# Optimization experiments

Measured on AMD Instinct MI355X. Metric: run time of the kernel, lower is better.

Reference implementation:

```python
import jax, jax.numpy as jnp
import numpy as np

N = 50000
E = 600000
D_IN = 128
HID = 128
OUT = 64


def setup_inputs() -> dict:
    key = jax.random.key(0)
    ks = jax.random.split(key, 12)
    x = jax.random.normal(ks[0], (N, D_IN), dtype=jnp.float32)
    edge_index = jax.random.randint(ks[1], (2, E), 0, N, dtype=jnp.int32)
    def lin(k, fan_in, fan_out):
        lim = 1.0 / np.sqrt(fan_in)
        kw, kb = jax.random.split(k)
        W = jax.random.uniform(kw, (fan_in, fan_out), minval=-lim, maxval=lim, dtype=jnp.float32)
        b = jax.random.uniform(kb, (fan_out,), minval=-lim, maxval=lim, dtype=jnp.float32)
        return W, b
    W1, b1 = lin(ks[2], D_IN, HID)
    W2, b2 = lin(ks[3], HID, HID)
    W3, b3 = lin(ks[4], HID, HID)
    fcW, fcb = lin(ks[5], HID, OUT)
    return {"x": x, "edge_index": edge_index, "W1": W1, "b1": b1,
            "W2": W2, "b2": b2, "W3": W3, "b3": b3, "fcW": fcW, "fcb": fcb}


def _gcn_prep(edge_index):
    # add self loops, compute symmetric normalization deg^-1/2 * deg^-1/2
    loop = jnp.arange(N, dtype=edge_index.dtype)
    src = jnp.concatenate([edge_index[0], loop])
    dst = jnp.concatenate([edge_index[1], loop])
    deg = jax.ops.segment_sum(jnp.ones_like(dst, dtype=jnp.float32), dst, num_segments=N)
    dinv = jnp.where(deg > 0, jax.lax.rsqrt(deg), 0.0)
    norm = dinv[src] * dinv[dst]  # [E+N]
    return src, dst, norm


def _gcn_layer(x, src, dst, norm, W, b):
    h = x @ W                      # [N, F_out]
    msg = h[src] * norm[:, None]   # gather + scale, [E+N, F_out]
    agg = jax.ops.segment_sum(msg, dst, num_segments=N)
    return agg + b


def reference(x, edge_index, W1, b1, W2, b2, W3, b3, fcW, fcb):
    src, dst, norm = _gcn_prep(edge_index)
    x = jax.nn.relu(_gcn_layer(x, src, dst, norm, W1, b1))
    x = jax.nn.relu(_gcn_layer(x, src, dst, norm, W2, b2))
    x = jax.nn.relu(_gcn_layer(x, src, dst, norm, W3, b3))
    virtual_node_embedding = x[-1]  # last node's embedding [HID]
    out = virtual_node_embedding @ fcW + fcb  # [OUT]
    return out
```

## Files before the change

kernel.cpp:

```cpp
#include <hip/hip_runtime.h>

#define NF 128
#define OUTF 64

#define M2 1
#define M1 2
#define M0 4

#define CAP_F2 2048
#define CAP_E3 4096
#define CAP_F1 32768
#define CAP_E2 65536
#define CAP_F0 131072
#define CAP_E1 262144


__global__ void k_seed(int* __restrict__ mark, int* __restrict__ F2,
                       int* __restrict__ cnt, int last) {
    if (threadIdx.x == 0) {
        mark[last] = M2;
        F2[0] = last;
        cnt[0] = 1;
    }
}

__global__ void k_mark(const int* __restrict__ src, const int* __restrict__ dst, int E,
                       int* __restrict__ mark, int checkBit, int setBit, int last,
                       int2* __restrict__ Elist, int Ecap, int* __restrict__ eCnt,
                       int* __restrict__ Flist, int Fcap, int* __restrict__ fCnt,
                       const int* __restrict__ selfList, const int* __restrict__ selfCnt,
                       int selfCap)
{
    int i = blockIdx.x * blockDim.x + threadIdx.x;

    if (selfList) {
        int sc = *selfCnt; if (sc > selfCap) sc = selfCap;
        if (i < sc) {
            int v = selfList[i];
            if (!(atomicOr(&mark[v], setBit) & setBit)) {
                int p = atomicAdd(fCnt, 1);
                if (p < Fcap) Flist[p] = v;
            }
        }
    }
    if (i < E) {
        int d = dst[i];
        bool hit = checkBit ? ((mark[d] & checkBit) != 0) : (d == last);
        if (hit) {
            int s = src[i];
            int p = atomicAdd(eCnt, 1);
            if (p < Ecap) Elist[p] = make_int2(s, d);
            if (!(atomicOr(&mark[s], setBit) & setBit)) {
                int q = atomicAdd(fCnt, 1);
                if (q < Fcap) Flist[q] = s;
            }
        }
    }
}

__global__ void k_degm(const int* __restrict__ dst, const int* __restrict__ mark,
                       int* __restrict__ deg, int E) {
    int i = blockIdx.x * blockDim.x + threadIdx.x;
    if (i < E) {
        int d = dst[i];
        if (mark[d]) atomicAdd(&deg[d], 1);
    }
}

__global__ void k_dinvm(const int* __restrict__ mark, const int* __restrict__ deg,
                        float* __restrict__ dinv, int n) {
    int i = blockIdx.x * blockDim.x + threadIdx.x;
    if (i < n && mark[i]) dinv[i] = rsqrtf(1.0f + (float)deg[i]);
}

__global__ __launch_bounds__(256) void k_gemm_rows(
    const int* __restrict__ list, const int* __restrict__ cntPtr, int cap,
    const float* __restrict__ Xin, const float* __restrict__ bias,
    const float* __restrict__ W, const float* __restrict__ dinv,
    const int* __restrict__ mark, int aggBit, int last,
    float* __restrict__ H, float* __restrict__ AGG)
{
    __shared__ float wsm[128][128];
    const int t = threadIdx.x;

    {
        const float4* W4 = (const float4*)W;
        float4* S4 = (float4*)&wsm[0][0];
        #pragma unroll
        for (int it = 0; it < 16; ++it) S4[it * 256 + t] = W4[it * 256 + t];
    }
    __syncthreads();

    int cnt = *cntPtr; if (cnt > cap) cnt = cap;
    const int wave = t >> 6, lane = t & 63;

    for (int base = blockIdx.x * 4; base < cnt; base += gridDim.x * 4) {
        int r = base + wave;
        if (r >= cnt) continue;
        int v = list[r];
        size_t off = (size_t)v * NF;

        float x0, x1;
        if (bias) {
            x0 = fmaxf(Xin[off + lane]      + bias[lane],      0.f);
            x1 = fmaxf(Xin[off + lane + 64] + bias[lane + 64], 0.f);
        } else {
            x0 = Xin[off + lane];
            x1 = Xin[off + lane + 64];
        }

        float a0 = 0.f, a1 = 0.f;
        #pragma unroll 16
        for (int k = 0; k < 64; ++k) {
            float xk = __shfl(x0, k);
            a0 += xk * wsm[k][lane];
            a1 += xk * wsm[k][lane + 64];
        }
        #pragma unroll 16
        for (int k = 0; k < 64; ++k) {
            float xk = __shfl(x1, k);
            a0 += xk * wsm[k + 64][lane];
            a1 += xk * wsm[k + 64][lane + 64];
        }

        H[off + lane]      = a0;
        H[off + lane + 64] = a1;

        bool doAgg = (mark ? ((mark[v] & aggBit) != 0) : false) || (v == last);
        if (doAgg) {
            float di = dinv[v], s2 = di * di;
            AGG[off + lane]      = a0 * s2;
            AGG[off + lane + 64] = a1 * s2;
        }
    }
}

__global__ void k_scat(const int2* __restrict__ list, const int* __restrict__ cntPtr, int cap,
                       const float* __restrict__ dinv, const float* __restrict__ H,
                       float* __restrict__ AGG)
{
    int cnt = *cntPtr; if (cnt > cap) cnt = cap;
    int t = threadIdx.x;
    for (int i = blockIdx.x; i < cnt; i += gridDim.x) {
        int2 e = list[i];
        float w = dinv[e.x] * dinv[e.y];
        atomicAdd(&AGG[(size_t)e.y * NF + t], H[(size_t)e.x * NF + t] * w);
    }
}

__global__ void k_fc(const float* __restrict__ AGG3, const float* __restrict__ b3,
                     const float* __restrict__ fcW, const float* __restrict__ fcb,
                     float* __restrict__ out, int last)
{
    __shared__ float xrow[NF];
    int j = threadIdx.x;
    size_t off = (size_t)last * NF;
    xrow[j]      = fmaxf(AGG3[off + j]      + b3[j],      0.f);
    xrow[j + 64] = fmaxf(AGG3[off + j + 64] + b3[j + 64], 0.f);
    __syncthreads();
    float acc = fcb[j];
    #pragma unroll 16
    for (int k = 0; k < NF; ++k) acc += xrow[k] * fcW[k * OUTF + j];
    out[j] = acc;
}

extern "C" void kernel_launch(void* const* d_in, const int* in_sizes, int n_in,
                              void* d_out, int out_size, void* d_ws, size_t ws_size,
                              hipStream_t stream)
{
    const float* x    = (const float*)d_in[0];
    const int*   ei   = (const int*)d_in[1];
    const float* W1   = (const float*)d_in[2];
    const float* b1   = (const float*)d_in[3];
    const float* W2   = (const float*)d_in[4];
    const float* b2   = (const float*)d_in[5];
    const float* W3   = (const float*)d_in[6];
    const float* b3   = (const float*)d_in[7];
    const float* fcW  = (const float*)d_in[8];
    const float* fcb  = (const float*)d_in[9];
    float* out = (float*)d_out;

    const int n = in_sizes[0] / NF;
    const int E = in_sizes[1] / 2;
    const int* src = ei;
    const int* dst = ei + E;
    const int last = n - 1;

    char* wp = (char*)d_ws;
    auto alloc = [&](size_t bytes) -> void* {
        void* r = (void*)wp;
        wp += (bytes + 255) & ~(size_t)255;
        return r;
    };
    int*   deg  = (int*)alloc((size_t)n * 4);
    int*   mark = (int*)alloc((size_t)n * 4);
    int*   cnt  = (int*)alloc(64 * 4);
    size_t zbytes = (char*)wp - (char*)deg;

    float* dinv = (float*)alloc((size_t)n * 4);
    int*   F2   = (int*) alloc(CAP_F2 * 4);
    int2*  E3   = (int2*)alloc(CAP_E3 * 8);
    int*   F1   = (int*) alloc(CAP_F1 * 4);
    int2*  E2   = (int2*)alloc(CAP_E2 * 8);
    int*   F0   = (int*) alloc(CAP_F0 * 4);
    int2*  E1   = (int2*)alloc(CAP_E1 * 8);
    float* H    = (float*)alloc((size_t)n * NF * 4);
    float* aggA = (float*)alloc((size_t)n * NF * 4);
    float* aggB = (float*)alloc((size_t)n * NF * 4);

    const int B  = 256;
    const int EB = (E + B - 1) / B;
    const int NB = (n + B - 1) / B;

    hipMemsetAsync(deg, 0, zbytes, stream);
    k_seed<<<1, 64, 0, stream>>>(mark, F2, cnt, last);

    k_mark<<<EB, B, 0, stream>>>(src, dst, E, mark, 0,  M2, last,
                                 E3, CAP_E3, &cnt[1], F2, CAP_F2, &cnt[0],
                                 nullptr, nullptr, 0);
    k_mark<<<EB, B, 0, stream>>>(src, dst, E, mark, M2, M1, last,
                                 E2, CAP_E2, &cnt[3], F1, CAP_F1, &cnt[2],
                                 F2, &cnt[0], CAP_F2);
    k_mark<<<EB, B, 0, stream>>>(src, dst, E, mark, M1, M0, last,
                                 E1, CAP_E1, &cnt[5], F0, CAP_F0, &cnt[4],
                                 F1, &cnt[2], CAP_F1);

    k_degm <<<EB, B, 0, stream>>>(dst, mark, deg, E);
    k_dinvm<<<NB, B, 0, stream>>>(mark, deg, dinv, n);

    k_gemm_rows<<<384, B, 0, stream>>>(F0, &cnt[4], CAP_F0, x, nullptr, W1,
                                       dinv, mark, M1, -1, H, aggA);
    k_scat<<<2048, 128, 0, stream>>>(E1, &cnt[5], CAP_E1, dinv, H, aggA);

    k_gemm_rows<<<384, B, 0, stream>>>(F1, &cnt[2], CAP_F1, aggA, b1, W2,
                                       dinv, mark, M2, -1, H, aggB);
    k_scat<<<2048, 128, 0, stream>>>(E2, &cnt[3], CAP_E2, dinv, H, aggB);

    k_gemm_rows<<<384, B, 0, stream>>>(F2, &cnt[0], CAP_F2, aggB, b2, W3,
                                       dinv, nullptr, 0, last, H, aggA);
    k_scat<<<2048, 128, 0, stream>>>(E3, &cnt[1], CAP_E3, dinv, H, aggA);

    k_fc<<<1, 64, 0, stream>>>(aggA, b3, fcW, fcb, out, last);
}
```

Measured before the change: 166.7 us.

## Fuse all GCN stages into one cooperative persistent kernel with grid syncs

Replaces the sequence of separate launches (memset, BFS marking, degree, gemm, scatter, fc) with a single cooperative kernel that separates the phases with grid-wide syncs. Degree counting is folded into the first BFS pass, dinv is recomputed on the fly with rsqrt instead of being stored, and the final layer plus the fc are done by one block without atomics. This removes per-launch overhead and the extra edge passes. In exchange, grid size is capped at 512 blocks, grid syncs add cost, and the layer-2 and layer-3 gemms read W from global memory instead of LDS.

Measured after the change: 623.4 us. 3.74x slower.

```diff
diff --git a/kernel.cpp b/kernel.cpp
--- a/kernel.cpp
+++ b/kernel.cpp
@@ -1,4 +1,7 @@
 #include <hip/hip_runtime.h>
+#include <hip/hip_cooperative_groups.h>
+
+namespace cg = cooperative_groups;
 
 #define NF 128
 #define OUTF 64
@@ -13,6 +16,243 @@
 #define CAP_E2 65536
 #define CAP_F0 131072
 #define CAP_E1 262144
+
+
+
+struct KArgs {
+    const float* x;
+    const int* srcp;
+    const int* dstp;
+    int E, n, last;
+    const float* W1; const float* b1;
+    const float* W2; const float* b2;
+    const float* W3; const float* b3;
+    const float* fcW; const float* fcb;
+    int* deg; int* mark; int* cnt;
+    int* F2; int2* E3l; int* F1; int2* E2l; int* F0; int2* E1l;
+    float* H; float* aggA; float* aggB;
+    float* out;
+};
+
+__device__ __forceinline__ void bfs_level(
+    const int* __restrict__ src, const int* __restrict__ dst, int E,
+    int* __restrict__ mark, int checkBit, int setBit,
+    int2* __restrict__ Elist, int Ecap, int* __restrict__ eCnt,
+    int* __restrict__ Flist, int Fcap, int* __restrict__ fCnt,
+    const int* __restrict__ selfList, int selfCnt,
+    int gtid, int gstride)
+{
+    for (int i = gtid; i < selfCnt; i += gstride) {
+        int v = selfList[i];
+        if (!(atomicOr(&mark[v], setBit) & setBit)) {
+            int p = atomicAdd(fCnt, 1);
+            if (p < Fcap) Flist[p] = v;
+        }
+    }
+    for (int i = gtid; i < E; i += gstride) {
+        int d = dst[i];
+        if (mark[d] & checkBit) {
+            int s = src[i];
+            int p = atomicAdd(eCnt, 1);
+            if (p < Ecap) Elist[p] = make_int2(s, d);
+            if (!(atomicOr(&mark[s], setBit) & setBit)) {
+                int q = atomicAdd(fCnt, 1);
+                if (q < Fcap) Flist[q] = s;
+            }
+        }
+    }
+}
+
+template<bool USE_LDS>
+__device__ __forceinline__ void gemm_phase(
+    const int* __restrict__ list, int rows,
+    const float* __restrict__ Xin, const float* __restrict__ bias,
+    const float* __restrict__ W, const int* __restrict__ deg,
+    const int* __restrict__ mark, int aggBit,
+    float* __restrict__ H, float* __restrict__ AGG,
+    float (&wsm)[128][128])
+{
+    if ((int)blockIdx.x * 4 >= rows) return;
+    const int t = threadIdx.x;
+    if (USE_LDS) {
+        const float4* W4 = (const float4*)W;
+        float4* S4 = (float4*)&wsm[0][0];
+        #pragma unroll
+        for (int it = 0; it < 16; ++it) S4[it * 256 + t] = W4[it * 256 + t];
+        __syncthreads();
+    }
+    const int wave = t >> 6, lane = t & 63;
+    for (int base = blockIdx.x * 4; base < rows; base += gridDim.x * 4) {
+        int r = base + wave;
+        if (r >= rows) continue;
+        int v = list[r];
+        size_t off = (size_t)v * NF;
+
+        float x0, x1;
+        if (bias) {
+            x0 = fmaxf(Xin[off + lane]      + bias[lane],      0.f);
+            x1 = fmaxf(Xin[off + lane + 64] + bias[lane + 64], 0.f);
+        } else {
+            x0 = Xin[off + lane];
+            x1 = Xin[off + lane + 64];
+        }
+
+        float a0 = 0.f, a1 = 0.f;
+        if (USE_LDS) {
+            #pragma unroll 16
+            for (int k = 0; k < 64; ++k) {
+                float xk = __shfl(x0, k);
+                a0 += xk * wsm[k][lane];
+                a1 += xk * wsm[k][lane + 64];
+            }
+            #pragma unroll 16
+            for (int k = 0; k < 64; ++k) {
+                float xk = __shfl(x1, k);
+                a0 += xk * wsm[k + 64][lane];
+                a1 += xk * wsm[k + 64][lane + 64];
+            }
+        } else {
+            #pragma unroll 8
+            for (int k = 0; k < 64; ++k) {
+                float xk = __shfl(x0, k);
+                a0 += xk * W[k * NF + lane];
+                a1 += xk * W[k * NF + lane + 64];
+            }
+            #pragma unroll 8
+            for (int k = 0; k < 64; ++k) {
+                float xk = __shfl(x1, k);
+                a0 += xk * W[(k + 64) * NF + lane];
+                a1 += xk * W[(k + 64) * NF + lane + 64];
+            }
+        }
+
+        H[off + lane]      = a0;
+        H[off + lane + 64] = a1;
+
+        if (mark[v] & aggBit) {
+            float di = rsqrtf(1.0f + (float)deg[v]);
+            float s2 = di * di;
+            AGG[off + lane]      = a0 * s2;
+            AGG[off + lane + 64] = a1 * s2;
+        }
+    }
+}
+
+__device__ __forceinline__ void scat_phase(
+    const int2* __restrict__ Elist, int ecnt,
+    const int* __restrict__ deg, const float* __restrict__ H,
+    float* __restrict__ AGG, int gtid, int gstride)
+{
+    int grp = gtid >> 7, f = gtid & 127, ngrp = gstride >> 7;
+    for (int i = grp; i < ecnt; i += ngrp) {
+        int2 e = Elist[i];
+        float w = rsqrtf(1.f + (float)deg[e.x]) * rsqrtf(1.f + (float)deg[e.y]);
+        atomicAdd(&AGG[(size_t)e.y * NF + f], H[(size_t)e.x * NF + f] * w);
+    }
+}
+
+__global__ __launch_bounds__(256, 2) void k_fused(KArgs a)
+{
+    __shared__ float wsm[128][128];
+    cg::grid_group grid = cg::this_grid();
+    const int gtid = blockIdx.x * blockDim.x + threadIdx.x;
+    const int gstride = gridDim.x * blockDim.x;
+    const int E = a.E, n = a.n, last = a.last;
+
+    for (int i = gtid; i < n; i += gstride) { a.deg[i] = 0; a.mark[i] = 0; }
+    if (gtid < 64) a.cnt[gtid] = 0;
+    grid.sync();
+
+    if (gtid == 0) {
+        if (!(atomicOr(&a.mark[last], M2) & M2)) {
+            int p = atomicAdd(&a.cnt[0], 1);
+            if (p < CAP_F2) a.F2[p] = last;
+        }
+    }
+    for (int i = gtid; i < E; i += gstride) {
+        int d = a.dstp[i];
+        atomicAdd(&a.deg[d], 1);
+        if (d == last) {
+            int s = a.srcp[i];
+            int p = atomicAdd(&a.cnt[1], 1);
+            if (p < CAP_E3) a.E3l[p] = make_int2(s, d);
+            if (!(atomicOr(&a.mark[s], M2) & M2)) {
+                int q = atomicAdd(&a.cnt[0], 1);
+                if (q < CAP_F2) a.F2[q] = s;
+            }
+        }
+    }
+    grid.sync();
+
+    bfs_level(a.srcp, a.dstp, E, a.mark, M2, M1,
+              a.E2l, CAP_E2, &a.cnt[3], a.F1, CAP_F1, &a.cnt[2],
+              a.F2, min(a.cnt[0], CAP_F2), gtid, gstride);
+    grid.sync();
+
+    bfs_level(a.srcp, a.dstp, E, a.mark, M1, M0,
+              a.E1l, CAP_E1, &a.cnt[5], a.F0, CAP_F0, &a.cnt[4],
+              a.F1, min(a.cnt[2], CAP_F1), gtid, gstride);
+    grid.sync();
+
+    gemm_phase<true>(a.F0, min(a.cnt[4], CAP_F0), a.x, nullptr, a.W1,
+                     a.deg, a.mark, M1, a.H, a.aggA, wsm);
+    grid.sync();
+
+    scat_phase(a.E1l, min(a.cnt[5], CAP_E1), a.deg, a.H, a.aggA, gtid, gstride);
+    grid.sync();
+
+    gemm_phase<false>(a.F1, min(a.cnt[2], CAP_F1), a.aggA, a.b1, a.W2,
+                      a.deg, a.mark, M2, a.H, a.aggB, wsm);
+    grid.sync();
+
+    scat_phase(a.E2l, min(a.cnt[3], CAP_E2), a.deg, a.H, a.aggB, gtid, gstride);
+    grid.sync();
+
+    if (blockIdx.x == 0) {
+        const int t = threadIdx.x;
+        const int wave = t >> 6, lane = t & 63;
+        int rows = min(a.cnt[0], CAP_F2);
+        for (int r = wave; r < rows; r += 4) {
+            int v = a.F2[r];
+            size_t off = (size_t)v * NF;
+            float x0 = fmaxf(a.aggB[off + lane]      + a.b2[lane],      0.f);
+            float x1 = fmaxf(a.aggB[off + lane + 64] + a.b2[lane + 64], 0.f);
+            float a0 = 0.f, a1 = 0.f;
+            #pragma unroll 8
+            for (int k = 0; k < 64; ++k) {
+                float xk = __shfl(x0, k);
+                a0 += xk * a.W3[k * NF + lane];
+                a1 += xk * a.W3[k * NF + lane + 64];
+            }
+            #pragma unroll 8
+            for (int k = 0; k < 64; ++k) {
+                float xk = __shfl(x1, k);
+                a0 += xk * a.W3[(k + 64) * NF + lane];
+                a1 += xk * a.W3[(k + 64) * NF + lane + 64];
+            }
+            a.H[off + lane]      = a0;
+            a.H[off + lane + 64] = a1;
+        }
+        __syncthreads();
+        if (t < NF) {
+            float dl = rsqrtf(1.f + (float)a.deg[last]);
+            float acc = dl * dl * a.H[(size_t)last * NF + t];
+            int e3 = min(a.cnt[1], CAP_E3);
+            for (int i = 0; i < e3; ++i) {
+                int s = a.E3l[i].x;
+                acc += rsqrtf(1.f + (float)a.deg[s]) * dl * a.H[(size_t)s * NF + t];
+            }
+            wsm[0][t] = fmaxf(acc + a.b3[t], 0.f);
+        }
+        __syncthreads();
+        if (t < OUTF) {
+            float acc = a.fcb[t];
+            #pragma unroll 16
+            for (int k = 0; k < NF; ++k) acc += wsm[0][k] * a.fcW[k * OUTF + t];
+            a.out[t] = acc;
+        }
+    }
+}
 
 
 __global__ void k_seed(int* __restrict__ mark, int* __restrict__ F2,
@@ -163,6 +403,7 @@
     for (int k = 0; k < NF; ++k) acc += xrow[k] * fcW[k * OUTF + j];
     out[j] = acc;
 }
+
 
 extern "C" void kernel_launch(void* const* d_in, const int* in_sizes, int n_in,
                               void* d_out, int out_size, void* d_ws, size_t ws_size,
@@ -208,6 +449,34 @@
     float* aggA = (float*)alloc((size_t)n * NF * 4);
     float* aggB = (float*)alloc((size_t)n * NF * 4);
 
+    static int coopState = -2;
+    if (coopState != -1) {
+        if (coopState == -2) {
+            int perCU = 0;
+            if (hipOccupancyMaxActiveBlocksPerMultiprocessor(&perCU, k_fused, 256, 0)
+                    != hipSuccess || perCU < 1)
+                perCU = 1;
+            long g = (long)perCU * 256;
+            if (g > 512) g = 512;
+            coopState = (int)g;
+        }
+        KArgs ha;
+        ha.x = x; ha.srcp = src; ha.dstp = dst;
+        ha.E = E; ha.n = n; ha.last = last;
+        ha.W1 = W1; ha.b1 = b1; ha.W2 = W2; ha.b2 = b2;
+        ha.W3 = W3; ha.b3 = b3; ha.fcW = fcW; ha.fcb = fcb;
+        ha.deg = deg; ha.mark = mark; ha.cnt = cnt;
+        ha.F2 = F2; ha.E3l = E3; ha.F1 = F1; ha.E2l = E2; ha.F0 = F0; ha.E1l = E1;
+        ha.H = H; ha.aggA = aggA; ha.aggB = aggB; ha.out = out;
+
+        void* params[1] = { (void*)&ha };
+        hipError_t err = hipLaunchCooperativeKernel(k_fused, dim3(coopState), dim3(256),
+                                                    params, 0u, stream);
+        if (err == hipSuccess) return;
+        coopState = -1;
+        (void)hipGetLastError();
+    }
+
     const int B  = 256;
     const int EB = (E + B - 1) / B;
     const int NB = (n + B - 1) / B;
```
